# Performance work log

Measured on AMD Instinct MI355X. Metric: run time of the kernel, lower is better.

## Reference

```python
import jax, jax.numpy as jnp
import numpy as np

B, S, D = 8, 512, 768
H = 12          # attention heads
E = 14          # routed experts
K = 4           # top-k experts per sequence
HID = D * 2     # expert mlp hidden (mlp_ratio=2)
SH = D * 2 * 2  # shared expert hidden (mlp_ratio * n_shared_experts)
EPS = 1e-5


def _ln(x, g, b):
    m = x.mean(-1, keepdims=True)
    v = ((x - m) ** 2).mean(-1, keepdims=True)
    return (x - m) / jnp.sqrt(v + EPS) * g + b


def _gelu(x):
    return jax.nn.gelu(x, approximate=False)


def setup_inputs() -> dict:
    key = jax.random.key(0)
    ks = jax.random.split(key, 12)
    p = lambda k, shape: jax.random.normal(k, shape, jnp.float32) * 0.02
    z = lambda *shape: jnp.zeros(shape, jnp.float32)
    return {
        "x": jax.random.normal(ks[0], (B, S, D), jnp.float32),
        "ln1_g": jnp.ones((D,), jnp.float32), "ln1_b": z(D),
        "qkv_w": p(ks[1], (D, 3 * D)),
        "proj_w": p(ks[2], (D, D)), "proj_b": z(D),
        "ln2_g": jnp.ones((D,), jnp.float32), "ln2_b": z(D),
        "router_w1": p(ks[3], (D, D)), "router_b1": z(D),
        "router_w2": p(ks[4], (D, E)), "router_b2": z(E),
        "exp_w1": p(ks[5], (E, D, HID)), "exp_b1": z(E, HID),
        "exp_w2": p(ks[6], (E, HID, D)), "exp_b2": z(E, D),
        "sh_w1": p(ks[7], (D, SH)), "sh_b1": z(SH),
        "sh_w2": p(ks[8], (SH, D)), "sh_b2": z(D),
    }


def _forward(x, ln1_g, ln1_b, qkv_w, proj_w, proj_b, ln2_g, ln2_b,
             router_w1, router_b1, router_w2, router_b2,
             exp_w1, exp_b1, exp_w2, exp_b2,
             sh_w1, sh_b1, sh_w2, sh_b2):
    dh = D // H
    scale = dh ** -0.5
    # --- attention branch ---
    h1 = _ln(x, ln1_g, ln1_b)
    qkv = (h1 @ qkv_w).reshape(B, S, 3, H, dh)
    q = jnp.moveaxis(qkv[:, :, 0], 2, 1)  # [B,H,S,dh]
    k = jnp.moveaxis(qkv[:, :, 1], 2, 1)
    v = jnp.moveaxis(qkv[:, :, 2], 2, 1)
    att = jax.nn.softmax(jnp.einsum('bhqd,bhkd->bhqk', q, k) * scale, axis=-1)
    ao = jnp.einsum('bhqk,bhkd->bqhd', att, v).reshape(B, S, D) @ proj_w + proj_b
    x2 = x + ao
    # --- MoE branch ---
    h = _ln(x2, ln2_g, ln2_b)
    seq_repr = h.mean(axis=1)                                   # [B,D]
    logits = _gelu(seq_repr @ router_w1 + router_b1) @ router_w2 + router_b2  # [B,E]
    probs = jax.nn.softmax(logits, axis=-1)
    tw, ti = jax.lax.top_k(probs, K)                            # [B,K]
    tw = jax.nn.softmax(tw, axis=-1)                            # re-normalize top-k
    w = (jax.nn.one_hot(ti, E, dtype=tw.dtype) * tw[..., None]).sum(1)  # [B,E]
    # dense all-expert compute; zero weight off the top-k replicates masked routing
    hid = _gelu(jnp.einsum('bsd,edh->ebsh', h, exp_w1) + exp_b1[:, None, None, :])
    eo = jnp.einsum('ebsh,ehd->ebsd', hid, exp_w2) + exp_b2[:, None, None, :]
    y = jnp.einsum('ebsd,be->bsd', eo, w)
    # shared experts
    y = y + _gelu(h @ sh_w1 + sh_b1) @ sh_w2 + sh_b2
    return x2 + y  # ls2 is Identity (init_values=None); aux_loss=0 in eval


def reference(x, ln1_g, ln1_b, qkv_w, proj_w, proj_b, ln2_g, ln2_b,
              router_w1, router_b1, router_w2, router_b2,
              exp_w1, exp_b1, exp_w2, exp_b2,
              sh_w1, sh_b1, sh_w2, sh_b2):
    return _forward(x, ln1_g, ln1_b, qkv_w, proj_w, proj_b, ln2_g, ln2_b,
                    router_w1, router_b1, router_w2, router_b2,
                    exp_w1, exp_b1, exp_w2, exp_b2,
                    sh_w1, sh_b1, sh_w2, sh_b2)
```

## Files before the change

kernel.cpp:

```cpp
#include <hip/hip_runtime.h>
#include <hip/hip_bf16.h>


typedef _Float16 f16x8 __attribute__((ext_vector_type(8)));
typedef float f32x4 __attribute__((ext_vector_type(4)));
typedef _Float16 f16;

__device__ __forceinline__ float gelu_fast(float x) {
  const float k2l2e = 2.f * 0.7978845608028654f * 1.4426950408889634f;
  float u = (x + 0.044715f * x * x * x) * k2l2e;
  float t = exp2f(u);
  return x * (1.f - 1.f / (t + 1.f));
}

__device__ __forceinline__ f32x4 mfma16(f16x8 a, f16x8 b, f32x4 c) {
  return __builtin_amdgcn_mfma_f32_16x16x32_f16(a, b, c, 0, 0, 0);
}

#define ASYNC_CP16(g, l)                                            \
  __builtin_amdgcn_global_load_lds(                                 \
      (const __attribute__((address_space(1))) void*)(g),           \
      (__attribute__((address_space(3))) void*)(l), 16, 0, 0)

#define GEMM_CORE(AB, WB, KK)                                               \
  for (int k0 = 0; k0 < (KK); k0 += 32) {                                   \
    __syncthreads();                                                        \
    ASYNC_CP16(&(AB)[(long)fr * (KK) + k0 + fc],        &sA[f]);            \
    ASYNC_CP16(&(AB)[(long)(fr + 64) * (KK) + k0 + fc], &sA[f + 2048]);     \
    ASYNC_CP16(&(WB)[(long)fr * (KK) + k0 + fc],        &sB[f]);            \
    ASYNC_CP16(&(WB)[(long)(fr + 64) * (KK) + k0 + fc], &sB[f + 2048]);     \
    __syncthreads();                                                        \
    f16x8 av[4], bv[4];                                                     \
    _Pragma("unroll")                                                       \
    for (int i = 0; i < 4; i++)                                             \
      av[i] = *(const f16x8*)&sA[(wm + i * 16 + lr) * 32 + q4 * 8];         \
    _Pragma("unroll")                                                       \
    for (int j = 0; j < 4; j++)                                             \
      bv[j] = *(const f16x8*)&sB[(wn + j * 16 + lr) * 32 + q4 * 8];         \
    _Pragma("unroll")                                                       \
    for (int i = 0; i < 4; i++)                                             \
      _Pragma("unroll")                                                     \
      for (int j = 0; j < 4; j++) acc[i][j] = mfma16(av[i], bv[j], acc[i][j]); \
  }

__global__ __launch_bounds__(256) void ln_kernel(
    const float* __restrict__ x, const float* __restrict__ g,
    const float* __restrict__ bt, f16* __restrict__ out,
    float* __restrict__ mout, float* __restrict__ rout)
{
  const int row = blockIdx.x;
  const float* xr = x + (long)row * 768;
  const int t = threadIdx.x;
  float v0 = xr[t], v1 = xr[t + 256], v2 = xr[t + 512];
  __shared__ float sb[8];
  float s = v0 + v1 + v2;
  #pragma unroll
  for (int o = 32; o > 0; o >>= 1) s += __shfl_xor(s, o, 64);
  const int w = t >> 6;
  if ((t & 63) == 0) sb[w] = s;
  __syncthreads();
  const float mean = (sb[0] + sb[1] + sb[2] + sb[3]) * (1.0f / 768.0f);
  const float d0 = v0 - mean, d1 = v1 - mean, d2 = v2 - mean;
  float q = d0 * d0 + d1 * d1 + d2 * d2;
  #pragma unroll
  for (int o = 32; o > 0; o >>= 1) q += __shfl_xor(q, o, 64);
  if ((t & 63) == 0) sb[4 + w] = q;
  __syncthreads();
  const float var = (sb[4] + sb[5] + sb[6] + sb[7]) * (1.0f / 768.0f);
  const float rstd = rsqrtf(var + 1e-5f);
  f16* orow = out + (long)row * 768;
  orow[t]       = (f16)(d0 * rstd * g[t]       + bt[t]);
  orow[t + 256] = (f16)(d1 * rstd * g[t + 256] + bt[t + 256]);
  orow[t + 512] = (f16)(d2 * rstd * g[t + 512] + bt[t + 512]);
  if (t == 0) { mout[row] = mean; rout[row] = rstd; }
}

struct TransArgs {
  const float* src[6];
  f16* dst[6];
  int rows[6], cols[6];
  int start[7];
};

__global__ __launch_bounds__(256) void transpose_all(TransArgs ta) {
  const int bid = blockIdx.x;
  int m = 0;
  #pragma unroll
  for (int i = 1; i < 6; i++) if (bid >= ta.start[i]) m = i;
  const int rows = ta.rows[m], cols = ta.cols[m];
  const int tilesC = cols >> 5;
  const int perB = (rows >> 5) * tilesC;
  int local = bid - ta.start[m];
  const int z = local / perB; local -= z * perB;
  const int tr = local / tilesC, tc = local - tr * tilesC;
  const float* inb = ta.src[m] + (long)z * rows * cols;
  f16* outb = ta.dst[m] + (long)z * rows * cols;
  const int c0 = tc * 32, r0 = tr * 32;
  __shared__ float tile[32][33];
  const int tx = threadIdx.x & 31, ty = threadIdx.x >> 5;
  #pragma unroll
  for (int i = 0; i < 32; i += 8)
    tile[ty + i][tx] = inb[(long)(r0 + ty + i) * cols + c0 + tx];
  __syncthreads();
  #pragma unroll
  for (int i = 0; i < 32; i += 8)
    outb[(long)(c0 + ty + i) * rows + r0 + tx] = (f16)tile[tx][ty + i];
}

#define EPI_QKV     0
#define EPI_RESID   1

template <int EPI>
__global__ __launch_bounds__(256) void gemm_bt(
    const f16* __restrict__ A, int K, long strideA, int aShift,
    const f16* __restrict__ W, long strideW,
    const float* __restrict__ bias, int strideBias,
    const int* __restrict__ topkIdx,
    void* __restrict__ outv, long strideOut, int ldout,
    const float* __restrict__ resid)
{
  __shared__ f16 sA[128 * 32];
  __shared__ f16 sB[128 * 32];
  const int tid = threadIdx.x;
  const int pair = blockIdx.z;
  const int m0 = blockIdx.y * 128;
  const int n0 = blockIdx.x * 128;
  const f16* Ab = A + ((long)(pair >> aShift)) * strideA + (long)m0 * K;
  const int wsel = topkIdx ? topkIdx[pair] : pair;
  const f16* Wb = W + (long)wsel * strideW + (long)n0 * K;

  const int f = tid * 8;
  const int fr = f >> 5;
  const int fc = f & 31;
  const int lane = tid & 63, wid = tid >> 6;
  const int wm = (wid >> 1) * 64, wn = (wid & 1) * 64;
  const int lr = lane & 15, q4 = lane >> 4;

  f32x4 zero = {0.f, 0.f, 0.f, 0.f};
  f32x4 acc[4][4];
  #pragma unroll
  for (int i = 0; i < 4; i++)
    #pragma unroll
    for (int j = 0; j < 4; j++) acc[i][j] = zero;

  GEMM_CORE(Ab, Wb, K);

  #pragma unroll
  for (int i = 0; i < 4; i++) {
    #pragma unroll
    for (int j = 0; j < 4; j++) {
      #pragma unroll
      for (int r = 0; r < 4; r++) {
        const int row = m0 + wm + i * 16 + q4 * 4 + r;
        const int col = n0 + wn + j * 16 + lr;
        float v = acc[i][j][r];
        if constexpr (EPI == EPI_QKV) {
          f16* qb = (f16*)outv;
          const int i3 = col / 768;
          const int rem = col - i3 * 768;
          const int hh = rem >> 6, dd = rem & 63;
          const int bb = row >> 9, ss = row & 511;
          const long bh = bb * 12 + hh;
          if (i3 == 0)      qb[(bh * 512 + ss) * 64 + dd] = (f16)v;
          else if (i3 == 1) qb[3145728 + (bh * 512 + ss) * 64 + dd] = (f16)v;
          else              qb[6291456 + (bh * 64 + dd) * 512 + ss] = (f16)v;
        } else {
          float* ob = (float*)outv;
          v += bias[col];
          ob[(long)row * ldout + col] = resid[(long)row * ldout + col] + v;
        }
      }
    }
  }
}

__global__ __launch_bounds__(256) void gemm_ffn1(
    const f16* __restrict__ hbuf,
    const f16* __restrict__ shw1t, const float* __restrict__ shb1,
    const f16* __restrict__ ew1t,  const float* __restrict__ eb1,
    const int* __restrict__ topk,  const float* __restrict__ wslot,
    f16* __restrict__ shid, f16* __restrict__ hid)
{
  __shared__ f16 sA[128 * 32];
  __shared__ f16 sB[128 * 32];
  const int orig = blockIdx.x;
  const int xcd = orig & 7, slot = orig >> 3;

  const int tid = threadIdx.x;
  const int f = tid * 8;
  const int fr = f >> 5, fc = f & 31;
  const int lane = tid & 63, wid = tid >> 6;
  const int wm = (wid >> 1) * 64, wn = (wid & 1) * 64;
  const int lr = lane & 15, q4 = lane >> 4;

  const f16* Ab;
  const f16* Wb;
  const float* bp;
  f16* outp;
  int ldo;
  float wscale;

  if (slot < 96) {
    const int l = xcd * 96 + slot;
    const int bx = l % 24, by = l / 24;
    const int n0 = bx * 128, m0 = by * 128;
    Ab = hbuf + (long)m0 * 768;
    Wb = shw1t + (long)n0 * 768;
    bp = shb1 + n0;
    outp = shid + (long)m0 * 3072 + n0;
    ldo = 3072;
    wscale = 1.f;
  } else {
    const int l = xcd * 192 + (slot - 96);
    const int bx = l % 12;
    const int u = l / 12;
    const int by = u & 3, pair = u >> 2;
    const int wsel = topk[pair];
    const int n0 = bx * 128;
    const int m0g = (pair >> 2) * 512 + by * 128;
    Ab = hbuf + (long)m0g * 768;
    Wb = ew1t + (long)wsel * (1536L * 768) + (long)n0 * 768;
    bp = eb1 + (long)wsel * 1536 + n0;
    outp = hid + (long)pair * (512L * 1536) + (long)(by * 128) * 1536 + n0;
    ldo = 1536;
    wscale = wslot[pair];
  }

  f32x4 zero = {0.f, 0.f, 0.f, 0.f};
  f32x4 acc[4][4];
  #pragma unroll
  for (int i = 0; i < 4; i++)
    #pragma unroll
    for (int j = 0; j < 4; j++) acc[i][j] = zero;

  GEMM_CORE(Ab, Wb, 768);

  #pragma unroll
  for (int i = 0; i < 4; i++)
    #pragma unroll
    for (int j = 0; j < 4; j++)
      #pragma unroll
      for (int r = 0; r < 4; r++) {
        const int rr = wm + i * 16 + q4 * 4 + r;
        const int cc = wn + j * 16 + lr;
        float v = acc[i][j][r] + bp[cc];
        outp[(long)rr * ldo + cc] = (f16)(gelu_fast(v) * wscale);
      }
}

__global__ __launch_bounds__(256) void gemm_ffn2(
    const f16* __restrict__ shid, const f16* __restrict__ shw2t,
    const float* __restrict__ shb2, const float* __restrict__ x2,
    const f16* __restrict__ hid, const f16* __restrict__ ew2t,
    const float* __restrict__ eb2,
    const int* __restrict__ topk, const float* __restrict__ wslot,
    float* __restrict__ dout, f16* __restrict__ eo)
{
  __shared__ f16 sA[128 * 32];
  __shared__ f16 sB[128 * 32];
  const int orig = blockIdx.x;
  const int xcd = orig & 7, slot = orig >> 3;

  const int tid = threadIdx.x;
  const int f = tid * 8;
  const int fr = f >> 5, fc = f & 31;
  const int lane = tid & 63, wid = tid >> 6;
  const int wm = (wid >> 1) * 64, wn = (wid & 1) * 64;
  const int lr = lane & 15, q4 = lane >> 4;

  const bool shared_role = (slot < 24);
  const f16* Ab;
  const f16* Wb;
  int K, m0, n0, pair = 0, wsel = 0;

  if (shared_role) {
    const int l = xcd * 24 + slot;
    const int bx = l % 6, by = l / 6;
    n0 = bx * 128; m0 = by * 128;
    K = 3072;
    Ab = shid + (long)m0 * 3072;
    Wb = shw2t + (long)n0 * 3072;
  } else {
    const int l = xcd * 96 + (slot - 24);
    const int bx = l % 6;
    const int u = l / 6;
    const int by = u & 3; pair = u >> 2;
    wsel = topk[pair];
    n0 = bx * 128; m0 = by * 128;
    K = 1536;
    Ab = hid + (long)pair * (512L * 1536) + (long)m0 * 1536;
    Wb = ew2t + (long)wsel * (768L * 1536) + (long)n0 * 1536;
  }

  f32x4 zero = {0.f, 0.f, 0.f, 0.f};
  f32x4 acc[4][4];
  #pragma unroll
  for (int i = 0; i < 4; i++)
    #pragma unroll
    for (int j = 0; j < 4; j++) acc[i][j] = zero;

  GEMM_CORE(Ab, Wb, K);

  if (shared_role) {
    float* op = dout + (long)m0 * 768 + n0;
    const float* rp = x2 + (long)m0 * 768 + n0;
    const float* bp = shb2 + n0;
    #pragma unroll
    for (int i = 0; i < 4; i++)
      #pragma unroll
      for (int j = 0; j < 4; j++)
        #pragma unroll
        for (int r = 0; r < 4; r++) {
          const int rr = wm + i * 16 + q4 * 4 + r;
          const int cc = wn + j * 16 + lr;
          op[(long)rr * 768 + cc] = rp[(long)rr * 768 + cc] + acc[i][j][r] + bp[cc];
        }
  } else {
    const float wscale = wslot[pair];
    f16* op = eo + (long)pair * (512L * 768) + (long)m0 * 768 + n0;
    const float* bp = eb2 + (long)wsel * 768 + n0;
    #pragma unroll
    for (int i = 0; i < 4; i++)
      #pragma unroll
      for (int j = 0; j < 4; j++)
        #pragma unroll
        for (int r = 0; r < 4; r++) {
          const int rr = wm + i * 16 + q4 * 4 + r;
          const int cc = wn + j * 16 + lr;
          op[(long)rr * 768 + cc] = (f16)(acc[i][j][r] + wscale * bp[cc]);
        }
  }
}

__device__ __forceinline__ int pswz(int row, int col) {
  return row * 512 + (col ^ ((row & 7) << 3));
}

__global__ __launch_bounds__(256) void attn_kernel(
    const f16* __restrict__ Q, const f16* __restrict__ Kt,
    const f16* __restrict__ Vt, f16* __restrict__ AO)
{
  __shared__ f16 Ps[64 * 512];
  const int bh = blockIdx.x;
  const int qt = blockIdx.y;
  const int t = threadIdx.x;
  const int lane = t & 63, w = t >> 6;
  const int lr = lane & 15, q4 = lane >> 4;
  const int r0 = qt * 64 + w * 16;
  const int lrow0 = w * 16;
  const f16* Qh = Q + (long)bh * 512 * 64;
  const f16* Kh = Kt + (long)bh * 512 * 64;

  f32x4 zero = {0.f, 0.f, 0.f, 0.f};
  f32x4 acc[32];
  #pragma unroll
  for (int i = 0; i < 32; i++) acc[i] = zero;

  #pragma unroll
  for (int kk = 0; kk < 2; kk++) {
    f16x8 a = *(const f16x8*)&Qh[(r0 + lr) * 64 + kk * 32 + q4 * 8];
    #pragma unroll
    for (int nt = 0; nt < 32; nt++) {
      f16x8 b = *(const f16x8*)&Kh[(nt * 16 + lr) * 64 + kk * 32 + q4 * 8];
      acc[nt] = mfma16(a, b, acc[nt]);
    }
  }

  const float cscale = 0.125f * 1.44269504089f;
  #pragma unroll
  for (int r = 0; r < 4; r++) {
    float m = -1e30f;
    #pragma unroll
    for (int nt = 0; nt < 32; nt++) m = fmaxf(m, acc[nt][r]);
    #pragma unroll
    for (int o = 1; o < 16; o <<= 1) m = fmaxf(m, __shfl_xor(m, o, 64));
    float s = 0.f;
    #pragma unroll
    for (int nt = 0; nt < 32; nt++) {
      float e = exp2f((acc[nt][r] - m) * cscale);
      acc[nt][r] = e; s += e;
    }
    #pragma unroll
    for (int o = 1; o < 16; o <<= 1) s += __shfl_xor(s, o, 64);
    const float inv = 1.f / s;
    const int lrow = lrow0 + q4 * 4 + r;
    #pragma unroll
    for (int nt = 0; nt < 32; nt++)
      Ps[pswz(lrow, nt * 16 + lr)] = (f16)(acc[nt][r] * inv);
  }

  const f16* Vh = Vt + (long)bh * 64 * 512;
  f32x4 o4[4];
  #pragma unroll
  for (int i = 0; i < 4; i++) o4[i] = zero;
  #pragma unroll
  for (int kk = 0; kk < 16; kk++) {
    f16x8 a = *(const f16x8*)&Ps[pswz(lrow0 + lr, kk * 32 + q4 * 8)];
    #pragma unroll
    for (int nt = 0; nt < 4; nt++) {
      f16x8 b = *(const f16x8*)&Vh[(nt * 16 + lr) * 512 + kk * 32 + q4 * 8];
      o4[nt] = mfma16(a, b, o4[nt]);
    }
  }
  const int b_ = bh / 12, h_ = bh - b_ * 12;
  #pragma unroll
  for (int nt = 0; nt < 4; nt++)
    #pragma unroll
    for (int r = 0; r < 4; r++) {
      const int rowg = r0 + q4 * 4 + r;
      AO[((long)(b_ * 512 + rowg)) * 768 + h_ * 64 + nt * 16 + lr] = (f16)o4[nt][r];
    }
}

__global__ __launch_bounds__(256) void router_reduce(
    const float* __restrict__ x2, const float* __restrict__ lnm,
    const float* __restrict__ lnr, float* __restrict__ part)
{
  const int c = blockIdx.x, b = blockIdx.y, t = threadIdx.x;
  float a0 = 0.f, a1 = 0.f, a2 = 0.f;
  #pragma unroll 4
  for (int s = 0; s < 32; s++) {
    const long base = (long)b * 512 + c * 32 + s;
    const float m = lnm[base], r = lnr[base];
    const float* xr = x2 + base * 768;
    a0 += (xr[t] - m) * r;
    a1 += (xr[t + 256] - m) * r;
    a2 += (xr[t + 512] - m) * r;
  }
  float* pr = part + ((long)b * 16 + c) * 768;
  pr[t] = a0; pr[t + 256] = a1; pr[t + 512] = a2;
}

__global__ __launch_bounds__(256) void router_seq(
    const float* __restrict__ part, const float* __restrict__ g2,
    const float* __restrict__ b2ln, float* __restrict__ seqg)
{
  const int b = blockIdx.x, t = threadIdx.x;
  const float* pb = part + (long)b * 16 * 768;
  #pragma unroll
  for (int i = 0; i < 3; i++) {
    const int j = t + 256 * i;
    float a = 0.f;
    #pragma unroll
    for (int c = 0; c < 16; c++) a += pb[c * 768 + j];
    seqg[b * 768 + j] = a * (1.f / 512.f) * g2[j] + b2ln[j];
  }
}

__global__ __launch_bounds__(256) void router_mlp1(
    const float* __restrict__ seqg, const float* __restrict__ rw1,
    float* __restrict__ pmlp)
{
  const int c = blockIdx.x, b = blockIdx.y, t = threadIdx.x;
  const float* sq = seqg + b * 768 + c * 48;
  float a0 = 0.f, a1 = 0.f, a2 = 0.f;
  #pragma unroll 8
  for (int d = 0; d < 48; d++) {
    const float s = sq[d];
    const float* wr = rw1 + (long)(c * 48 + d) * 768;
    a0 += s * wr[t];
    a1 += s * wr[t + 256];
    a2 += s * wr[t + 512];
  }
  float* pr = pmlp + ((long)b * 16 + c) * 768;
  pr[t] = a0; pr[t + 256] = a1; pr[t + 512] = a2;
}

__global__ __launch_bounds__(256) void router_fold(
    const float* __restrict__ pmlp, const float* __restrict__ rb1,
    float* __restrict__ g1g)
{
  const int b = blockIdx.x, t = threadIdx.x;
  const float* pb = pmlp + (long)b * 16 * 768;
  #pragma unroll
  for (int i = 0; i < 3; i++) {
    const int j = t + 256 * i;
    float a = rb1[j];
    #pragma unroll
    for (int c = 0; c < 16; c++) a += pb[c * 768 + j];
    g1g[b * 768 + j] = 0.5f * a * (1.0f + erff(a * 0.70710678118654752f));
  }
}

__global__ __launch_bounds__(256) void router_top(
    const float* __restrict__ g1g, const float* __restrict__ rw2,
    const float* __restrict__ rb2, float* __restrict__ wslot,
    int* __restrict__ topkIdx)
{
  __shared__ float lg[14];
  const int b = blockIdx.x, t = threadIdx.x;
  const int e = t >> 4, sub = t & 15;
  if (e < 14) {
    float a = 0.f;
    #pragma unroll
    for (int i = 0; i < 48; i++) {
      const int d = sub + 16 * i;
      a += g1g[b * 768 + d] * rw2[d * 14 + e];
    }
    #pragma unroll
    for (int o = 1; o < 16; o <<= 1) a += __shfl_xor(a, o, 64);
    if (sub == 0) lg[e] = a + rb2[e];
  }
  __syncthreads();
  if (t == 0) {
    float mx = -1e30f;
    for (int ee = 0; ee < 14; ee++) mx = fmaxf(mx, lg[ee]);
    float p[14], s = 0.f;
    for (int ee = 0; ee < 14; ee++) { p[ee] = expf(lg[ee] - mx); s += p[ee]; }
    for (int ee = 0; ee < 14; ee++) p[ee] /= s;
    int idx[4]; float val[4]; bool used[14];
    for (int ee = 0; ee < 14; ee++) used[ee] = false;
    for (int k = 0; k < 4; k++) {
      int best = -1; float bv = -1.f;
      for (int ee = 0; ee < 14; ee++)
        if (!used[ee] && p[ee] > bv) { bv = p[ee]; best = ee; }
      used[best] = true; idx[k] = best; val[k] = bv;
    }
    const float m2 = val[0];
    float ss = 0.f, e4[4];
    for (int k = 0; k < 4; k++) { e4[k] = expf(val[k] - m2); ss += e4[k]; }
    for (int k = 0; k < 4; k++) {
      wslot[b * 4 + k] = e4[k] / ss;
      topkIdx[b * 4 + k] = idx[k];
    }
  }
}

__global__ __launch_bounds__(256) void combine_kernel(
    const f16* __restrict__ eo, float* __restrict__ out)
{
  const long i = (long)blockIdx.x * 256 + threadIdx.x;
  const long b = i / (512L * 768);
  const long loc = i - b * (512L * 768);
  const f16* e0 = eo + b * 4 * (512L * 768) + loc;
  float v = out[i];
  v += (float)e0[0] + (float)e0[512L * 768] + (float)e0[2 * 512L * 768] +
       (float)e0[3 * 512L * 768];
  out[i] = v;
}

static const long OFF_X2    = 0L;
static const long OFF_LNM   = 12582912L;
static const long OFF_LNR   = OFF_LNM + 16384L;
static const long OFF_WSLOT = OFF_LNR + 16384L;
static const long OFF_TOPK  = OFF_WSLOT + 256L;
static const long OFF_PART  = OFF_TOPK + 256L;
static const long OFF_SEQG  = OFF_PART + 393216L;
static const long OFF_PMLP  = OFF_SEQG + 24576L;
static const long OFF_G1G   = OFF_PMLP + 393216L;
static const long W_QKVWT  = 13631488L;
static const long W_PROJWT = W_QKVWT + 3538944L;
static const long W_EW1T   = W_PROJWT + 1179648L;
static const long W_EW2T   = W_EW1T + 33030144L;
static const long W_SHW1T  = W_EW2T + 33030144L;
static const long W_SHW2T  = W_SHW1T + 4718592L;
static const long OFF_ACT  = 93847552L;
static const long A_H1     = OFF_ACT;
static const long A_Q      = OFF_ACT + 6291456L;
static const long A_AO     = A_Q + 18874368L;
static const long B_H      = OFF_ACT;
static const long B_HID    = OFF_ACT + 6291456L;
static const long B_SHID   = B_HID + 50331648L;
static const long B_EO     = B_SHID + 25165824L;

extern "C" void kernel_launch(void* const* d_in, const int* in_sizes, int n_in,
                              void* d_out, int out_size, void* d_ws, size_t ws_size,
                              hipStream_t stream) {
  const float* x     = (const float*)d_in[0];
  const float* ln1g  = (const float*)d_in[1];
  const float* ln1b  = (const float*)d_in[2];
  const float* qkvw  = (const float*)d_in[3];
  const float* projw = (const float*)d_in[4];
  const float* projb = (const float*)d_in[5];
  const float* ln2g  = (const float*)d_in[6];
  const float* ln2b  = (const float*)d_in[7];
  const float* rw1   = (const float*)d_in[8];
  const float* rb1   = (const float*)d_in[9];
  const float* rw2   = (const float*)d_in[10];
  const float* rb2   = (const float*)d_in[11];
  const float* ew1   = (const float*)d_in[12];
  const float* eb1   = (const float*)d_in[13];
  const float* ew2   = (const float*)d_in[14];
  const float* eb2   = (const float*)d_in[15];
  const float* shw1  = (const float*)d_in[16];
  const float* shb1  = (const float*)d_in[17];
  const float* shw2  = (const float*)d_in[18];
  const float* shb2  = (const float*)d_in[19];

  char* ws = (char*)d_ws;
  float* x2    = (float*)(ws + OFF_X2);
  float* lnm   = (float*)(ws + OFF_LNM);
  float* lnr   = (float*)(ws + OFF_LNR);
  float* wslot = (float*)(ws + OFF_WSLOT);
  int*   topk  = (int*)(ws + OFF_TOPK);
  float* part  = (float*)(ws + OFF_PART);
  float* seqg  = (float*)(ws + OFF_SEQG);
  float* pmlp  = (float*)(ws + OFF_PMLP);
  float* g1g   = (float*)(ws + OFF_G1G);
  f16* qkvwt  = (f16*)(ws + W_QKVWT);
  f16* projwt = (f16*)(ws + W_PROJWT);
  f16* ew1t   = (f16*)(ws + W_EW1T);
  f16* ew2t   = (f16*)(ws + W_EW2T);
  f16* shw1t  = (f16*)(ws + W_SHW1T);
  f16* shw2t  = (f16*)(ws + W_SHW2T);
  f16* h1     = (f16*)(ws + A_H1);
  f16* Qb     = (f16*)(ws + A_Q);
  f16* aob    = (f16*)(ws + A_AO);
  f16* hbuf   = (f16*)(ws + B_H);
  f16* hid    = (f16*)(ws + B_HID);
  f16* shid   = (f16*)(ws + B_SHID);
  f16* eo     = (f16*)(ws + B_EO);

  TransArgs ta;
  ta.src[0] = qkvw;  ta.dst[0] = qkvwt;  ta.rows[0] = 768;  ta.cols[0] = 2304;
  ta.src[1] = projw; ta.dst[1] = projwt; ta.rows[1] = 768;  ta.cols[1] = 768;
  ta.src[2] = ew1;   ta.dst[2] = ew1t;   ta.rows[2] = 768;  ta.cols[2] = 1536;
  ta.src[3] = ew2;   ta.dst[3] = ew2t;   ta.rows[3] = 1536; ta.cols[3] = 768;
  ta.src[4] = shw1;  ta.dst[4] = shw1t;  ta.rows[4] = 768;  ta.cols[4] = 3072;
  ta.src[5] = shw2;  ta.dst[5] = shw2t;  ta.rows[5] = 3072; ta.cols[5] = 768;
  ta.start[0] = 0;     ta.start[1] = 1728;  ta.start[2] = 2304;
  ta.start[3] = 18432; ta.start[4] = 34560; ta.start[5] = 36864;
  ta.start[6] = 39168;
  transpose_all<<<39168, 256, 0, stream>>>(ta);

  ln_kernel<<<4096, 256, 0, stream>>>(x, ln1g, ln1b, h1, lnm, lnr);
  gemm_bt<EPI_QKV><<<dim3(18, 32, 1), 256, 0, stream>>>(
      h1, 768, 0, 0, qkvwt, 0, nullptr, 0, nullptr, (void*)Qb, 0, 0, nullptr);
  attn_kernel<<<dim3(96, 8, 1), 256, 0, stream>>>(Qb, Qb + 3145728, Qb + 6291456, aob);
  gemm_bt<EPI_RESID><<<dim3(6, 32, 1), 256, 0, stream>>>(
      aob, 768, 0, 0, projwt, 0, projb, 0, nullptr, (void*)x2, 0, 768, x);

  ln_kernel<<<4096, 256, 0, stream>>>(x2, ln2g, ln2b, hbuf, lnm, lnr);
  router_reduce<<<dim3(16, 8, 1), 256, 0, stream>>>(x2, lnm, lnr, part);
  router_seq<<<8, 256, 0, stream>>>(part, ln2g, ln2b, seqg);
  router_mlp1<<<dim3(16, 8, 1), 256, 0, stream>>>(seqg, rw1, pmlp);
  router_fold<<<8, 256, 0, stream>>>(pmlp, rb1, g1g);
  router_top<<<8, 256, 0, stream>>>(g1g, rw2, rb2, wslot, topk);
  gemm_ffn1<<<2304, 256, 0, stream>>>(hbuf, shw1t, shb1, ew1t, eb1,
                                      topk, wslot, shid, hid);
  gemm_ffn2<<<960, 256, 0, stream>>>(shid, shw2t, shb2, x2, hid, ew2t, eb2,
                                     topk, wslot, (float*)d_out, eo);
  combine_kernel<<<12288, 256, 0, stream>>>(eo, (float*)d_out);
}
```

Before: 600.8 us.

## Split-K the FFN2 GEMMs and reduce partials in the combine kernel

The second FFN GEMM now splits K: the shared expert into 4 chunks of 768 and each routed expert into 2 chunks, so the grid grows from 960 to 2304 blocks. Before, the grid had fewer blocks and long K loops, which left CUs underused. Each chunk writes an fp16 partial to a workspace buffer. The combine kernel then sums the 4 shared partials and 8 expert partials, adding the residual and the shared bias. This gains parallelism at the cost of much more intermediate memory traffic and some extra fp16 rounding of the partials.

```diff
diff --git a/kernel.cpp b/kernel.cpp
--- a/kernel.cpp
+++ b/kernel.cpp
@@ -22,13 +22,13 @@
       (const __attribute__((address_space(1))) void*)(g),           \
       (__attribute__((address_space(3))) void*)(l), 16, 0, 0)
 
-#define GEMM_CORE(AB, WB, KK)                                               \
+#define GEMM_CORE(AB, WB, LDA, LDB, KK)                                     \
   for (int k0 = 0; k0 < (KK); k0 += 32) {                                   \
     __syncthreads();                                                        \
-    ASYNC_CP16(&(AB)[(long)fr * (KK) + k0 + fc],        &sA[f]);            \
-    ASYNC_CP16(&(AB)[(long)(fr + 64) * (KK) + k0 + fc], &sA[f + 2048]);     \
-    ASYNC_CP16(&(WB)[(long)fr * (KK) + k0 + fc],        &sB[f]);            \
-    ASYNC_CP16(&(WB)[(long)(fr + 64) * (KK) + k0 + fc], &sB[f + 2048]);     \
+    ASYNC_CP16(&(AB)[(long)fr * (LDA) + k0 + fc],        &sA[f]);           \
+    ASYNC_CP16(&(AB)[(long)(fr + 64) * (LDA) + k0 + fc], &sA[f + 2048]);    \
+    ASYNC_CP16(&(WB)[(long)fr * (LDB) + k0 + fc],        &sB[f]);           \
+    ASYNC_CP16(&(WB)[(long)(fr + 64) * (LDB) + k0 + fc], &sB[f + 2048]);    \
     __syncthreads();                                                        \
     f16x8 av[4], bv[4];                                                     \
     _Pragma("unroll")                                                       \
@@ -143,7 +143,7 @@
     #pragma unroll
     for (int j = 0; j < 4; j++) acc[i][j] = zero;
 
-  GEMM_CORE(Ab, Wb, K);
+  GEMM_CORE(Ab, Wb, K, K, K);
 
   #pragma unroll
   for (int i = 0; i < 4; i++) {
@@ -233,7 +233,7 @@
     #pragma unroll
     for (int j = 0; j < 4; j++) acc[i][j] = zero;
 
-  GEMM_CORE(Ab, Wb, 768);
+  GEMM_CORE(Ab, Wb, 768, 768, 768);
 
   #pragma unroll
   for (int i = 0; i < 4; i++)
@@ -250,11 +250,10 @@
 
 __global__ __launch_bounds__(256) void gemm_ffn2(
     const f16* __restrict__ shid, const f16* __restrict__ shw2t,
-    const float* __restrict__ shb2, const float* __restrict__ x2,
     const f16* __restrict__ hid, const f16* __restrict__ ew2t,
     const float* __restrict__ eb2,
     const int* __restrict__ topk, const float* __restrict__ wslot,
-    float* __restrict__ dout, f16* __restrict__ eo)
+    f16* __restrict__ sp, f16* __restrict__ eo)
 {
   __shared__ f16 sA[128 * 32];
   __shared__ f16 sB[128 * 32];
@@ -268,28 +267,42 @@
   const int wm = (wid >> 1) * 64, wn = (wid & 1) * 64;
   const int lr = lane & 15, q4 = lane >> 4;
 
-  const bool shared_role = (slot < 24);
+  const bool shared_role = (slot < 96);
   const f16* Ab;
   const f16* Wb;
-  int K, m0, n0, pair = 0, wsel = 0;
+  long ld;
+  f16* op;
+  const float* bp = nullptr;
+  float wscale = 0.f;
+  int kc;
 
   if (shared_role) {
-    const int l = xcd * 24 + slot;
-    const int bx = l % 6, by = l / 6;
-    n0 = bx * 128; m0 = by * 128;
-    K = 3072;
-    Ab = shid + (long)m0 * 3072;
-    Wb = shw2t + (long)n0 * 3072;
+    const int l = xcd * 96 + slot;
+    const int mt = l / 24;
+    const int r = l - mt * 24;
+    const int nt = r >> 2;
+    kc = r & 3;
+    const int m0 = mt * 128, n0 = nt * 128, k0 = kc * 768;
+    ld = 3072;
+    Ab = shid + (long)m0 * 3072 + k0;
+    Wb = shw2t + (long)n0 * 3072 + k0;
+    op = sp + (long)kc * (4096L * 768) + (long)m0 * 768 + n0;
   } else {
-    const int l = xcd * 96 + (slot - 24);
-    const int bx = l % 6;
-    const int u = l / 6;
-    const int by = u & 3; pair = u >> 2;
-    wsel = topk[pair];
-    n0 = bx * 128; m0 = by * 128;
-    K = 1536;
-    Ab = hid + (long)pair * (512L * 1536) + (long)m0 * 1536;
-    Wb = ew2t + (long)wsel * (768L * 1536) + (long)n0 * 1536;
+    const int l = xcd * 192 + (slot - 96);
+    const int pair = l / 48;
+    const int r = l - pair * 48;
+    const int mt = r / 12;
+    const int r2 = r - mt * 12;
+    const int nt = r2 >> 1;
+    kc = r2 & 1;
+    const int wsel = topk[pair];
+    const int m0 = mt * 128, n0 = nt * 128, k0 = kc * 768;
+    ld = 1536;
+    Ab = hid + (long)pair * (512L * 1536) + (long)m0 * 1536 + k0;
+    Wb = ew2t + (long)wsel * (768L * 1536) + (long)n0 * 1536 + k0;
+    op = eo + (long)(pair * 2 + kc) * (512L * 768) + (long)m0 * 768 + n0;
+    bp = eb2 + (long)wsel * 768 + n0;
+    wscale = wslot[pair];
   }
 
   f32x4 zero = {0.f, 0.f, 0.f, 0.f};
@@ -299,37 +312,21 @@
     #pragma unroll
     for (int j = 0; j < 4; j++) acc[i][j] = zero;
 
-  GEMM_CORE(Ab, Wb, K);
-
-  if (shared_role) {
-    float* op = dout + (long)m0 * 768 + n0;
-    const float* rp = x2 + (long)m0 * 768 + n0;
-    const float* bp = shb2 + n0;
-    #pragma unroll
-    for (int i = 0; i < 4; i++)
+  GEMM_CORE(Ab, Wb, ld, ld, 768);
+
+  const bool addb = (!shared_role) && (kc == 0);
+  #pragma unroll
+  for (int i = 0; i < 4; i++)
+    #pragma unroll
+    for (int j = 0; j < 4; j++)
       #pragma unroll
-      for (int j = 0; j < 4; j++)
-        #pragma unroll
-        for (int r = 0; r < 4; r++) {
-          const int rr = wm + i * 16 + q4 * 4 + r;
-          const int cc = wn + j * 16 + lr;
-          op[(long)rr * 768 + cc] = rp[(long)rr * 768 + cc] + acc[i][j][r] + bp[cc];
-        }
-  } else {
-    const float wscale = wslot[pair];
-    f16* op = eo + (long)pair * (512L * 768) + (long)m0 * 768 + n0;
-    const float* bp = eb2 + (long)wsel * 768 + n0;
-    #pragma unroll
-    for (int i = 0; i < 4; i++)
-      #pragma unroll
-      for (int j = 0; j < 4; j++)
-        #pragma unroll
-        for (int r = 0; r < 4; r++) {
-          const int rr = wm + i * 16 + q4 * 4 + r;
-          const int cc = wn + j * 16 + lr;
-          op[(long)rr * 768 + cc] = (f16)(acc[i][j][r] + wscale * bp[cc]);
-        }
-  }
+      for (int r = 0; r < 4; r++) {
+        const int rr = wm + i * 16 + q4 * 4 + r;
+        const int cc = wn + j * 16 + lr;
+        float v = acc[i][j][r];
+        if (addb) v += wscale * bp[cc];
+        op[(long)rr * 768 + cc] = (f16)v;
+      }
 }
 
 __device__ __forceinline__ int pswz(int row, int col) {
@@ -527,15 +524,21 @@
 }
 
 __global__ __launch_bounds__(256) void combine_kernel(
-    const f16* __restrict__ eo, float* __restrict__ out)
+    const f16* __restrict__ eo, const f16* __restrict__ sp,
+    const float* __restrict__ x2, const float* __restrict__ shb2,
+    float* __restrict__ out)
 {
   const long i = (long)blockIdx.x * 256 + threadIdx.x;
   const long b = i / (512L * 768);
   const long loc = i - b * (512L * 768);
-  const f16* e0 = eo + b * 4 * (512L * 768) + loc;
-  float v = out[i];
-  v += (float)e0[0] + (float)e0[512L * 768] + (float)e0[2 * 512L * 768] +
-       (float)e0[3 * 512L * 768];
+  const long row = loc / 768;
+  const int col = (int)(loc - row * 768);
+  float v = x2[i] + shb2[col];
+  #pragma unroll
+  for (int k = 0; k < 4; k++) v += (float)sp[k * (4096L * 768) + i];
+  const f16* e0 = eo + b * 8 * (512L * 768) + loc;
+  #pragma unroll
+  for (int s = 0; s < 8; s++) v += (float)e0[s * (512L * 768)];
   out[i] = v;
 }
 
@@ -562,6 +565,7 @@
 static const long B_HID    = OFF_ACT + 6291456L;
 static const long B_SHID   = B_HID + 50331648L;
 static const long B_EO     = B_SHID + 25165824L;
+static const long B_SP     = B_EO + 50331648L;
 
 extern "C" void kernel_launch(void* const* d_in, const int* in_sizes, int n_in,
                               void* d_out, int out_size, void* d_ws, size_t ws_size,
@@ -610,6 +614,7 @@
   f16* hid    = (f16*)(ws + B_HID);
   f16* shid   = (f16*)(ws + B_SHID);
   f16* eo     = (f16*)(ws + B_EO);
+  f16* sp     = (f16*)(ws + B_SP);
 
   TransArgs ta;
   ta.src[0] = qkvw;  ta.dst[0] = qkvwt;  ta.rows[0] = 768;  ta.cols[0] = 2304;
@@ -638,7 +643,7 @@
   router_top<<<8, 256, 0, stream>>>(g1g, rw2, rb2, wslot, topk);
   gemm_ffn1<<<2304, 256, 0, stream>>>(hbuf, shw1t, shb1, ew1t, eb1,
                                       topk, wslot, shid, hid);
-  gemm_ffn2<<<960, 256, 0, stream>>>(shid, shw2t, shb2, x2, hid, ew2t, eb2,
-                                     topk, wslot, (float*)d_out, eo);
-  combine_kernel<<<12288, 256, 0, stream>>>(eo, (float*)d_out);
-}
+  gemm_ffn2<<<2304, 256, 0, stream>>>(shid, shw2t, hid, ew2t, eb2,
+                                      topk, wslot, sp, eo);
+  combine_kernel<<<12288, 256, 0, stream>>>(eo, sp, x2, shb2, (float*)d_out);
+}
```

Result: slower. 624.7 us (+4.0%).

## Double-buffer LDS tiles in GEMM core to overlap async loads with MFMA

Applied to the files above, without the earlier changes.

The GEMM main loop now uses two LDS buffers per operand, issuing the async global-to-LDS copy for the next K-slice before running the MFMAs on the current one, with one barrier per iteration instead of two. This is meant to hide global load latency behind the matrix math. The FFN2 kernel also splits into two specialised calls with compile-time K, so each loop has a constant trip count. In exchange, LDS use per block doubles to 32KB, which may lower occupancy, and there is more code.

```diff
diff --git a/kernel.cpp b/kernel.cpp
--- a/kernel.cpp
+++ b/kernel.cpp
@@ -22,25 +22,35 @@
       (const __attribute__((address_space(1))) void*)(g),           \
       (__attribute__((address_space(3))) void*)(l), 16, 0, 0)
 
-#define GEMM_CORE(AB, WB, KK)                                               \
-  for (int k0 = 0; k0 < (KK); k0 += 32) {                                   \
-    __syncthreads();                                                        \
-    ASYNC_CP16(&(AB)[(long)fr * (KK) + k0 + fc],        &sA[f]);            \
-    ASYNC_CP16(&(AB)[(long)(fr + 64) * (KK) + k0 + fc], &sA[f + 2048]);     \
-    ASYNC_CP16(&(WB)[(long)fr * (KK) + k0 + fc],        &sB[f]);            \
-    ASYNC_CP16(&(WB)[(long)(fr + 64) * (KK) + k0 + fc], &sB[f + 2048]);     \
-    __syncthreads();                                                        \
-    f16x8 av[4], bv[4];                                                     \
-    _Pragma("unroll")                                                       \
-    for (int i = 0; i < 4; i++)                                             \
-      av[i] = *(const f16x8*)&sA[(wm + i * 16 + lr) * 32 + q4 * 8];         \
-    _Pragma("unroll")                                                       \
-    for (int j = 0; j < 4; j++)                                             \
-      bv[j] = *(const f16x8*)&sB[(wn + j * 16 + lr) * 32 + q4 * 8];         \
-    _Pragma("unroll")                                                       \
-    for (int i = 0; i < 4; i++)                                             \
-      _Pragma("unroll")                                                     \
-      for (int j = 0; j < 4; j++) acc[i][j] = mfma16(av[i], bv[j], acc[i][j]); \
+#define GEMM_STAGE(AB, WB, LDA, LDB, koff, buf)                               \
+  ASYNC_CP16(&(AB)[(long)fr * (LDA) + (koff) + fc],        &sA[(buf) * 4096 + f]);        \
+  ASYNC_CP16(&(AB)[(long)(fr + 64) * (LDA) + (koff) + fc], &sA[(buf) * 4096 + f + 2048]); \
+  ASYNC_CP16(&(WB)[(long)fr * (LDB) + (koff) + fc],        &sB[(buf) * 4096 + f]);        \
+  ASYNC_CP16(&(WB)[(long)(fr + 64) * (LDB) + (koff) + fc], &sB[(buf) * 4096 + f + 2048]);
+
+#define GEMM_CORE(AB, WB, LDA, LDB, KK)                                       \
+  {                                                                           \
+    GEMM_STAGE(AB, WB, LDA, LDB, 0, 0)                                        \
+    __syncthreads();                                                          \
+    int cur = 0;                                                              \
+    for (int k0 = 0; k0 < (KK); k0 += 32) {                                   \
+      f16x8 av[4], bv[4];                                                     \
+      _Pragma("unroll")                                                       \
+      for (int i = 0; i < 4; i++)                                             \
+        av[i] = *(const f16x8*)&sA[cur * 4096 + (wm + i * 16 + lr) * 32 + q4 * 8]; \
+      _Pragma("unroll")                                                       \
+      for (int j = 0; j < 4; j++)                                             \
+        bv[j] = *(const f16x8*)&sB[cur * 4096 + (wn + j * 16 + lr) * 32 + q4 * 8]; \
+      if (k0 + 32 < (KK)) {                                                   \
+        GEMM_STAGE(AB, WB, LDA, LDB, k0 + 32, cur ^ 1)                        \
+      }                                                                       \
+      _Pragma("unroll")                                                       \
+      for (int i = 0; i < 4; i++)                                             \
+        _Pragma("unroll")                                                     \
+        for (int j = 0; j < 4; j++) acc[i][j] = mfma16(av[i], bv[j], acc[i][j]); \
+      if (k0 + 32 < (KK)) __syncthreads();                                    \
+      cur ^= 1;                                                               \
+    }                                                                         \
   }
 
 __global__ __launch_bounds__(256) void ln_kernel(
@@ -119,8 +129,8 @@
     void* __restrict__ outv, long strideOut, int ldout,
     const float* __restrict__ resid)
 {
-  __shared__ f16 sA[128 * 32];
-  __shared__ f16 sB[128 * 32];
+  __shared__ f16 sA[2 * 128 * 32];
+  __shared__ f16 sB[2 * 128 * 32];
   const int tid = threadIdx.x;
   const int pair = blockIdx.z;
   const int m0 = blockIdx.y * 128;
@@ -143,7 +153,7 @@
     #pragma unroll
     for (int j = 0; j < 4; j++) acc[i][j] = zero;
 
-  GEMM_CORE(Ab, Wb, K);
+  GEMM_CORE(Ab, Wb, K, K, K);
 
   #pragma unroll
   for (int i = 0; i < 4; i++) {
@@ -181,8 +191,8 @@
     const int* __restrict__ topk,  const float* __restrict__ wslot,
     f16* __restrict__ shid, f16* __restrict__ hid)
 {
-  __shared__ f16 sA[128 * 32];
-  __shared__ f16 sB[128 * 32];
+  __shared__ f16 sA[2 * 128 * 32];
+  __shared__ f16 sB[2 * 128 * 32];
   const int orig = blockIdx.x;
   const int xcd = orig & 7, slot = orig >> 3;
 
@@ -233,7 +243,7 @@
     #pragma unroll
     for (int j = 0; j < 4; j++) acc[i][j] = zero;
 
-  GEMM_CORE(Ab, Wb, 768);
+  GEMM_CORE(Ab, Wb, 768, 768, 768);
 
   #pragma unroll
   for (int i = 0; i < 4; i++)
@@ -256,8 +266,8 @@
     const int* __restrict__ topk, const float* __restrict__ wslot,
     float* __restrict__ dout, f16* __restrict__ eo)
 {
-  __shared__ f16 sA[128 * 32];
-  __shared__ f16 sB[128 * 32];
+  __shared__ f16 sA[2 * 128 * 32];
+  __shared__ f16 sB[2 * 128 * 32];
   const int orig = blockIdx.x;
   const int xcd = orig & 7, slot = orig >> 3;
 
@@ -299,7 +309,11 @@
     #pragma unroll
     for (int j = 0; j < 4; j++) acc[i][j] = zero;
 
-  GEMM_CORE(Ab, Wb, K);
+  if (shared_role) {
+    GEMM_CORE(Ab, Wb, 3072, 3072, 3072);
+  } else {
+    GEMM_CORE(Ab, Wb, 1536, 1536, 1536);
+  }
 
   if (shared_role) {
     float* op = dout + (long)m0 * 768 + n0;
```

Result: faster. 588.2 us (-2.1%).
